# Kernel optimization log

Measured on AMD Instinct MI355X. Metric: run time of the kernel, lower is better.

## Reference

```python
import jax, jax.numpy as jnp
import numpy as np

LN_EPS = 1e-5


def setup_inputs() -> dict:
    key = jax.random.key(0)
    ks = jax.random.split(key, 6)
    B, S, Dv, Dk, A = 32, 2048, 1024, 1024, 1024
    meta_state = jax.random.normal(ks[0], (B, S, Dv), dtype=jnp.float32)
    hidden_previous = jax.random.normal(ks[1], (B, Dk), dtype=jnp.float32)
    # torch nn.Linear weights are [out_features, in_features]
    WK = jax.random.normal(ks[2], (A, Dv), dtype=jnp.float32) * (1.0 / np.sqrt(Dv))
    WQ = jax.random.normal(ks[3], (A, Dk), dtype=jnp.float32) * (1.0 / np.sqrt(Dk))
    WV = jax.random.normal(ks[4], (Dv, Dv), dtype=jnp.float32) * (1.0 / np.sqrt(Dv))
    WO = jax.random.normal(ks[5], (Dv, Dv), dtype=jnp.float32) * (1.0 / np.sqrt(Dv))
    ln_w = jnp.ones((Dv,), dtype=jnp.float32)
    ln_b = jnp.zeros((Dv,), dtype=jnp.float32)
    return {"meta_state": meta_state, "hidden_previous": hidden_previous,
            "WK": WK, "WQ": WQ, "WV": WV, "WO": WO, "ln_w": ln_w, "ln_b": ln_b}


def reference(meta_state, hidden_previous, WK, WQ, WV, WO, ln_w, ln_b):
    A = WK.shape[0]
    scale = 1.0 / jnp.sqrt(jnp.asarray(A, dtype=meta_state.dtype))
    # projections
    K = jnp.einsum('bsd,ad->bsa', meta_state, WK)          # [B,S,A]
    q = jnp.einsum('bd,ad->ba', hidden_previous, WQ)       # [B,A]
    V = jnp.einsum('bsd,ed->bse', meta_state, WV)          # [B,S,Dv]
    # single-query attention over sequence dim
    logits = jnp.einsum('bsa,ba->bs', K, q) * scale        # [B,S]
    weight = jax.nn.softmax(logits, axis=1)                # softmax over S (dim=1)
    attention = jnp.einsum('bse,bs->be', V, weight)        # [B,Dv]
    # output layer: Linear(no bias) -> Tanh -> LayerNorm (dropout = identity in eval)
    h = jnp.tanh(attention @ WO.T)
    mu = jnp.mean(h, axis=-1, keepdims=True)
    var = jnp.mean(jnp.square(h - mu), axis=-1, keepdims=True)
    out = (h - mu) / jnp.sqrt(var + LN_EPS) * ln_w + ln_b  # [B,Dv]
    return out, weight[..., None]                          # weight shape [B,S,1] as in torch
```

## Files before the change

### kernel.cpp

```cpp
#include <hip/hip_runtime.h>
#include <math.h>

#define B 32
#define S 2048
#define D 1024
#define CPB 64
#define CHROWS (S / CPB)
#define WROWS (CHROWS / 4)
#define ACH 16
#define SCALE (1.0f / 32.0f)
#define LN_EPS 1e-5f

__device__ __forceinline__ float wave_sum(float v) {
#pragma unroll
  for (int off = 32; off > 0; off >>= 1) v += __shfl_xor(v, off, 64);
  return v;
}

__global__ __launch_bounds__(256) void gemm_xw(const float* __restrict__ X,
                                               const float* __restrict__ W,
                                               float* __restrict__ Y,
                                               const int do_tanh) {
  const int t = threadIdx.x;
  const int b = t & 31;
  const int rr = (t >> 5) & 3;
  const int kh = t >> 7;
  const int r = blockIdx.x * 4 + rr;
  const float4* x4 = (const float4*)(X + (size_t)b * D + kh * (D / 2));
  const float4* w4 = (const float4*)(W + (size_t)r * D + kh * (D / 2));
  float acc = 0.f;
#pragma unroll 8
  for (int k = 0; k < D / 8; ++k) {
    float4 a = x4[k];
    float4 w = w4[k];
    acc += a.x * w.x + a.y * w.y + a.z * w.z + a.w * w.w;
  }
  __shared__ float part[256];
  part[t] = acc;
  __syncthreads();
  if (kh == 0) {
    float v = part[t] + part[t + 128];
    if (do_tanh) v = tanhf(v);
    Y[(size_t)b * D + r] = v;
  }
}

__global__ __launch_bounds__(256) void kq_partial(const float* __restrict__ q,
                                                  const float* __restrict__ WK,
                                                  float* __restrict__ kqp) {
  const int t = threadIdx.x, ac = blockIdx.x, bg = blockIdx.y;
  const int d0 = t * 4;
  float accx[8] = {}, accy[8] = {}, accz[8] = {}, accw[8] = {};
  const int a0 = ac * (1024 / ACH);
  for (int a = a0; a < a0 + (1024 / ACH); ++a) {
    float4 wk = *(const float4*)(WK + (size_t)a * D + d0);
#pragma unroll
    for (int j = 0; j < 8; ++j) {
      float qv = q[(size_t)(bg * 8 + j) * D + a];
      accx[j] += qv * wk.x;
      accy[j] += qv * wk.y;
      accz[j] += qv * wk.z;
      accw[j] += qv * wk.w;
    }
  }
#pragma unroll
  for (int j = 0; j < 8; ++j) {
    float4 o;
    o.x = accx[j]; o.y = accy[j]; o.z = accz[j]; o.w = accw[j];
    *(float4*)(kqp + ((size_t)ac * B + bg * 8 + j) * D + d0) = o;
  }
}

__global__ __launch_bounds__(64) void kq_reduce(const float* __restrict__ kqp,
                                                float* __restrict__ kq) {
  const int i4 = (blockIdx.x * 64 + threadIdx.x) * 4;
  float sx = 0.f, sy = 0.f, sz = 0.f, sw = 0.f;
  for (int c = 0; c < ACH; ++c) {
    float4 v = *(const float4*)(kqp + (size_t)c * (B * D) + i4);
    sx += v.x; sy += v.y; sz += v.z; sw += v.w;
  }
  float4 o;
  o.x = sx; o.y = sy; o.z = sz; o.w = sw;
  *(float4*)(kq + i4) = o;
}

__global__ __launch_bounds__(256) void attn_main(
    const float* __restrict__ meta, const float* __restrict__ kq,
    float* __restrict__ logits_out, float* __restrict__ cm,
    float* __restrict__ cl, float* __restrict__ cacc) {
  const int c = blockIdx.x, b = blockIdx.y;
  const int t = threadIdx.x, w = t >> 6, lane = t & 63;
  const int row0 = c * CHROWS + w * WROWS;
  const float* base = meta + ((size_t)b * S + row0) * D + lane * 4;

  float4 kqf[4];
#pragma unroll
  for (int j = 0; j < 4; ++j)
    kqf[j] = *(const float4*)(kq + (size_t)b * D + j * 256 + lane * 4);

  float4 acc[4] = {};
  float m = -INFINITY, l = 0.f;

  float4 v[4], vn[4];
#pragma unroll
  for (int j = 0; j < 4; ++j) v[j] = *(const float4*)(base + j * 256);

  for (int s = 0; s < WROWS; ++s) {
    const float* nb = base + (size_t)(s + 1 < WROWS ? s + 1 : s) * D;
#pragma unroll
    for (int j = 0; j < 4; ++j) vn[j] = *(const float4*)(nb + j * 256);

    float p = 0.f;
#pragma unroll
    for (int j = 0; j < 4; ++j)
      p += v[j].x * kqf[j].x + v[j].y * kqf[j].y + v[j].z * kqf[j].z +
           v[j].w * kqf[j].w;
    p = wave_sum(p);
    const float logit = p * SCALE;
    if (lane == 0) logits_out[(size_t)b * S + row0 + s] = logit;

    if (logit > m) {
      const float f = expf(m - logit);
#pragma unroll
      for (int j = 0; j < 4; ++j) {
        acc[j].x *= f; acc[j].y *= f; acc[j].z *= f; acc[j].w *= f;
      }
      l *= f;
      m = logit;
    }
    const float p2 = expf(logit - m);
#pragma unroll
    for (int j = 0; j < 4; ++j) {
      acc[j].x += p2 * v[j].x; acc[j].y += p2 * v[j].y;
      acc[j].z += p2 * v[j].z; acc[j].w += p2 * v[j].w;
    }
    l += p2;
#pragma unroll
    for (int j = 0; j < 4; ++j) v[j] = vn[j];
  }

  __shared__ float lds_acc[4][D];
  __shared__ float lds_m[4], lds_l[4];
  if (lane == 0) { lds_m[w] = m; lds_l[w] = l; }
#pragma unroll
  for (int j = 0; j < 4; ++j)
    *(float4*)(&lds_acc[w][j * 256 + lane * 4]) = acc[j];
  __syncthreads();

  const float M = fmaxf(fmaxf(lds_m[0], lds_m[1]), fmaxf(lds_m[2], lds_m[3]));
  float fac[4], L = 0.f;
#pragma unroll
  for (int w2 = 0; w2 < 4; ++w2) {
    fac[w2] = expf(lds_m[w2] - M);
    L += lds_l[w2] * fac[w2];
  }
  float4 sv = {};
#pragma unroll
  for (int w2 = 0; w2 < 4; ++w2) {
    float4 a = *(const float4*)(&lds_acc[w2][t * 4]);
    sv.x += fac[w2] * a.x; sv.y += fac[w2] * a.y;
    sv.z += fac[w2] * a.z; sv.w += fac[w2] * a.w;
  }
  const int pc = b * CPB + c;
  *(float4*)(cacc + (size_t)pc * D + t * 4) = sv;
  if (t == 0) { cm[pc] = M; cl[pc] = L; }
}

__global__ __launch_bounds__(128) void combine(const float* __restrict__ cm,
                                               const float* __restrict__ cl,
                                               const float* __restrict__ cacc,
                                               float* __restrict__ wio,
                                               float* __restrict__ wm) {
  const int b = blockIdx.x, dt = blockIdx.y, t = threadIdx.x;
  float M = -INFINITY;
  for (int c2 = 0; c2 < CPB; ++c2) M = fmaxf(M, cm[b * CPB + c2]);
  __shared__ float fac[CPB];
  if (t < CPB) fac[t] = expf(cm[b * CPB + t] - M);
  __syncthreads();
  float L = 0.f;
  for (int c2 = 0; c2 < CPB; ++c2) L += cl[b * CPB + c2] * fac[c2];
  const float invL = 1.0f / L;

  const int d = dt * 128 + t;
  float sv = 0.f;
  for (int c2 = 0; c2 < CPB; ++c2)
    sv += fac[c2] * cacc[((size_t)b * CPB + c2) * D + d];
  wm[(size_t)b * D + d] = sv * invL;

  for (int s = dt * 256 + t; s < dt * 256 + 256; s += 128) {
    const float lg = wio[(size_t)b * S + s];
    wio[(size_t)b * S + s] = expf(lg - M) * invL;
  }
}

__global__ __launch_bounds__(256) void ln_kernel(const float* __restrict__ h,
                                                 const float* __restrict__ lnw,
                                                 const float* __restrict__ lnb,
                                                 float* __restrict__ out) {
  const int b = blockIdx.x, t = threadIdx.x, wid = t >> 6, lane = t & 63;
  __shared__ float r1[4], r2[4];
  float4 v = *(const float4*)(h + (size_t)b * D + 4 * t);
  float s1 = v.x + v.y + v.z + v.w;
  float s2 = v.x * v.x + v.y * v.y + v.z * v.z + v.w * v.w;
  s1 = wave_sum(s1);
  s2 = wave_sum(s2);
  if (lane == 0) { r1[wid] = s1; r2[wid] = s2; }
  __syncthreads();
  const float mean = (r1[0] + r1[1] + r1[2] + r1[3]) * (1.0f / D);
  const float ms = (r2[0] + r2[1] + r2[2] + r2[3]) * (1.0f / D);
  const float var = ms - mean * mean;
  const float rstd = rsqrtf(var + LN_EPS);
  float4 w = *(const float4*)(lnw + 4 * t);
  float4 bb = *(const float4*)(lnb + 4 * t);
  float4 o;
  o.x = (v.x - mean) * rstd * w.x + bb.x;
  o.y = (v.y - mean) * rstd * w.y + bb.y;
  o.z = (v.z - mean) * rstd * w.z + bb.z;
  o.w = (v.w - mean) * rstd * w.w + bb.w;
  *(float4*)(out + (size_t)b * D + 4 * t) = o;
}

extern "C" void kernel_launch(void* const* d_in, const int* in_sizes, int n_in,
                              void* d_out, int out_size, void* d_ws,
                              size_t ws_size, hipStream_t stream) {
  (void)in_sizes; (void)n_in; (void)out_size; (void)ws_size;
  const float* meta   = (const float*)d_in[0];
  const float* hidden = (const float*)d_in[1];
  const float* WK = (const float*)d_in[2];
  const float* WQ = (const float*)d_in[3];
  const float* WV = (const float*)d_in[4];
  const float* WO = (const float*)d_in[5];
  const float* lnw = (const float*)d_in[6];
  const float* lnb = (const float*)d_in[7];

  float* out  = (float*)d_out;
  float* wout = out + B * D;

  float* ws   = (float*)d_ws;
  float* q    = ws;
  float* kqp  = q + B * D;
  float* kq   = kqp + (size_t)ACH * B * D;
  float* cm   = kq + B * D;
  float* cl   = cm + B * CPB;
  float* cacc = cl + B * CPB;
  float* wm   = cacc + (size_t)B * CPB * D;
  float* att  = wm + B * D;
  float* h    = att + B * D;

  gemm_xw<<<dim3(D / 4), 256, 0, stream>>>(hidden, WQ, q, 0);
  kq_partial<<<dim3(ACH, 4), 256, 0, stream>>>(q, WK, kqp);
  kq_reduce<<<dim3((B * D) / 256), 64, 0, stream>>>(kqp, kq);
  attn_main<<<dim3(CPB, B), 256, 0, stream>>>(meta, kq, wout, cm, cl, cacc);
  combine<<<dim3(B, 8), 128, 0, stream>>>(cm, cl, cacc, wout, wm);
  gemm_xw<<<dim3(D / 4), 256, 0, stream>>>(wm, WV, att, 0);
  gemm_xw<<<dim3(D / 4), 256, 0, stream>>>(att, WO, h, 1);
  ln_kernel<<<dim3(B), 256, 0, stream>>>(h, lnw, lnb, out);
}
```

Before: 475.6 us.

## Fuse kq reduction into attention, unroll rows by two, restructure small GEMMs

Removes the separate kq_reduce kernel: each attention block now sums the 16 partial kq chunks itself and stages the result through shared memory. The attention loop handles two sequence rows per iteration, sharing one wave reduction and one max/rescale step, and fast __expf replaces expf. The small GEMM kernel is rewritten so each wave owns one batch row, keeps x in registers and streams 32 weight rows with prefetch. The trade-off is redundant kqp reads by every attention block (64 per batch), higher register use, and slightly less accurate exponentials.

```diff
diff --git a/kernel.cpp b/kernel.cpp
--- a/kernel.cpp
+++ b/kernel.cpp
@@ -17,31 +17,50 @@
   return v;
 }
 
+__device__ __forceinline__ void wave_sum2(float& a, float& b) {
+#pragma unroll
+  for (int off = 32; off > 0; off >>= 1) {
+    a += __shfl_xor(a, off, 64);
+    b += __shfl_xor(b, off, 64);
+  }
+}
+
 __global__ __launch_bounds__(256) void gemm_xw(const float* __restrict__ X,
                                                const float* __restrict__ W,
                                                float* __restrict__ Y,
                                                const int do_tanh) {
-  const int t = threadIdx.x;
-  const int b = t & 31;
-  const int rr = (t >> 5) & 3;
-  const int kh = t >> 7;
-  const int r = blockIdx.x * 4 + rr;
-  const float4* x4 = (const float4*)(X + (size_t)b * D + kh * (D / 2));
-  const float4* w4 = (const float4*)(W + (size_t)r * D + kh * (D / 2));
-  float acc = 0.f;
-#pragma unroll 8
-  for (int k = 0; k < D / 8; ++k) {
-    float4 a = x4[k];
-    float4 w = w4[k];
-    acc += a.x * w.x + a.y * w.y + a.z * w.z + a.w * w.w;
-  }
-  __shared__ float part[256];
-  part[t] = acc;
-  __syncthreads();
-  if (kh == 0) {
-    float v = part[t] + part[t + 128];
-    if (do_tanh) v = tanhf(v);
-    Y[(size_t)b * D + r] = v;
+  const int w = threadIdx.x >> 6, lane = threadIdx.x & 63;
+  const int b = blockIdx.x * 4 + w;
+  const int r0 = blockIdx.y * 32;
+
+  float4 x[4];
+  const float4* xrow = (const float4*)(X + (size_t)b * D) + lane;
+#pragma unroll
+  for (int j = 0; j < 4; ++j) x[j] = xrow[j * 64];
+
+  float4 wv[4], wn[4];
+  const float4* wrow = (const float4*)(W + (size_t)r0 * D) + lane;
+#pragma unroll
+  for (int j = 0; j < 4; ++j) wv[j] = wrow[j * 64];
+
+  for (int i = 0; i < 32; ++i) {
+    const float4* wnext =
+        (const float4*)(W + (size_t)(r0 + (i + 1 < 32 ? i + 1 : i)) * D) + lane;
+#pragma unroll
+    for (int j = 0; j < 4; ++j) wn[j] = wnext[j * 64];
+
+    float p = 0.f;
+#pragma unroll
+    for (int j = 0; j < 4; ++j)
+      p += x[j].x * wv[j].x + x[j].y * wv[j].y + x[j].z * wv[j].z +
+           x[j].w * wv[j].w;
+    p = wave_sum(p);
+    if (lane == 0) {
+      if (do_tanh) p = tanhf(p);
+      Y[(size_t)b * D + r0 + i] = p;
+    }
+#pragma unroll
+    for (int j = 0; j < 4; ++j) wv[j] = wn[j];
   }
 }
 
@@ -71,21 +90,8 @@
   }
 }
 
-__global__ __launch_bounds__(64) void kq_reduce(const float* __restrict__ kqp,
-                                                float* __restrict__ kq) {
-  const int i4 = (blockIdx.x * 64 + threadIdx.x) * 4;
-  float sx = 0.f, sy = 0.f, sz = 0.f, sw = 0.f;
-  for (int c = 0; c < ACH; ++c) {
-    float4 v = *(const float4*)(kqp + (size_t)c * (B * D) + i4);
-    sx += v.x; sy += v.y; sz += v.z; sw += v.w;
-  }
-  float4 o;
-  o.x = sx; o.y = sy; o.z = sz; o.w = sw;
-  *(float4*)(kq + i4) = o;
-}
-
 __global__ __launch_bounds__(256) void attn_main(
-    const float* __restrict__ meta, const float* __restrict__ kq,
+    const float* __restrict__ meta, const float* __restrict__ kqp,
     float* __restrict__ logits_out, float* __restrict__ cm,
     float* __restrict__ cl, float* __restrict__ cacc) {
   const int c = blockIdx.x, b = blockIdx.y;
@@ -93,54 +99,87 @@
   const int row0 = c * CHROWS + w * WROWS;
   const float* base = meta + ((size_t)b * S + row0) * D + lane * 4;
 
+  __shared__ float lds_acc[4][D];
+  __shared__ float lds_m[4], lds_l[4];
+  float* kq_lds = &lds_acc[0][0];
+
+  {
+    float sx = 0.f, sy = 0.f, sz = 0.f, sw = 0.f;
+#pragma unroll
+    for (int ch = 0; ch < ACH; ++ch) {
+      float4 kv = *(const float4*)(kqp + ((size_t)ch * B + b) * D + 4 * t);
+      sx += kv.x; sy += kv.y; sz += kv.z; sw += kv.w;
+    }
+    float4 o;
+    o.x = sx; o.y = sy; o.z = sz; o.w = sw;
+    *(float4*)(&kq_lds[4 * t]) = o;
+  }
+
+  float4 v0[4], v1[4];
+#pragma unroll
+  for (int j = 0; j < 4; ++j) {
+    v0[j] = *(const float4*)(base + j * 256);
+    v1[j] = *(const float4*)(base + D + j * 256);
+  }
+
+  __syncthreads();
   float4 kqf[4];
 #pragma unroll
   for (int j = 0; j < 4; ++j)
-    kqf[j] = *(const float4*)(kq + (size_t)b * D + j * 256 + lane * 4);
+    kqf[j] = *(const float4*)(&kq_lds[j * 256 + lane * 4]);
+  __syncthreads();
 
   float4 acc[4] = {};
   float m = -INFINITY, l = 0.f;
 
-  float4 v[4], vn[4];
-#pragma unroll
-  for (int j = 0; j < 4; ++j) v[j] = *(const float4*)(base + j * 256);
-
-  for (int s = 0; s < WROWS; ++s) {
-    const float* nb = base + (size_t)(s + 1 < WROWS ? s + 1 : s) * D;
-#pragma unroll
-    for (int j = 0; j < 4; ++j) vn[j] = *(const float4*)(nb + j * 256);
-
-    float p = 0.f;
-#pragma unroll
-    for (int j = 0; j < 4; ++j)
-      p += v[j].x * kqf[j].x + v[j].y * kqf[j].y + v[j].z * kqf[j].z +
-           v[j].w * kqf[j].w;
-    p = wave_sum(p);
-    const float logit = p * SCALE;
-    if (lane == 0) logits_out[(size_t)b * S + row0 + s] = logit;
-
-    if (logit > m) {
-      const float f = expf(m - logit);
+  for (int it = 0; it < WROWS / 2; ++it) {
+    const int nr = (it + 1 < WROWS / 2) ? 2 * it + 2 : 2 * it;
+    const float* nb = base + (size_t)nr * D;
+    float4 n0[4], n1[4];
+#pragma unroll
+    for (int j = 0; j < 4; ++j) {
+      n0[j] = *(const float4*)(nb + j * 256);
+      n1[j] = *(const float4*)(nb + D + j * 256);
+    }
+
+    float pa = 0.f, pb = 0.f;
+#pragma unroll
+    for (int j = 0; j < 4; ++j) {
+      pa += v0[j].x * kqf[j].x + v0[j].y * kqf[j].y + v0[j].z * kqf[j].z +
+            v0[j].w * kqf[j].w;
+      pb += v1[j].x * kqf[j].x + v1[j].y * kqf[j].y + v1[j].z * kqf[j].z +
+            v1[j].w * kqf[j].w;
+    }
+    wave_sum2(pa, pb);
+    const float la = pa * SCALE, lb = pb * SCALE;
+    if (lane == 0) {
+      logits_out[(size_t)b * S + row0 + 2 * it] = la;
+      logits_out[(size_t)b * S + row0 + 2 * it + 1] = lb;
+    }
+
+    const float mn = fmaxf(m, fmaxf(la, lb));
+    if (mn > m) {
+      const float f = __expf(m - mn);
 #pragma unroll
       for (int j = 0; j < 4; ++j) {
         acc[j].x *= f; acc[j].y *= f; acc[j].z *= f; acc[j].w *= f;
       }
       l *= f;
-      m = logit;
-    }
-    const float p2 = expf(logit - m);
+      m = mn;
+    }
+    const float ea = __expf(la - m), eb = __expf(lb - m);
 #pragma unroll
     for (int j = 0; j < 4; ++j) {
-      acc[j].x += p2 * v[j].x; acc[j].y += p2 * v[j].y;
-      acc[j].z += p2 * v[j].z; acc[j].w += p2 * v[j].w;
-    }
-    l += p2;
-#pragma unroll
-    for (int j = 0; j < 4; ++j) v[j] = vn[j];
-  }
-
-  __shared__ float lds_acc[4][D];
-  __shared__ float lds_m[4], lds_l[4];
+      acc[j].x += ea * v0[j].x + eb * v1[j].x;
+      acc[j].y += ea * v0[j].y + eb * v1[j].y;
+      acc[j].z += ea * v0[j].z + eb * v1[j].z;
+      acc[j].w += ea * v0[j].w + eb * v1[j].w;
+    }
+    l += ea + eb;
+#pragma unroll
+    for (int j = 0; j < 4; ++j) { v0[j] = n0[j]; v1[j] = n1[j]; }
+  }
+
   if (lane == 0) { lds_m[w] = m; lds_l[w] = l; }
 #pragma unroll
   for (int j = 0; j < 4; ++j)
@@ -151,7 +190,7 @@
   float fac[4], L = 0.f;
 #pragma unroll
   for (int w2 = 0; w2 < 4; ++w2) {
-    fac[w2] = expf(lds_m[w2] - M);
+    fac[w2] = __expf(lds_m[w2] - M);
     L += lds_l[w2] * fac[w2];
   }
   float4 sv = {};
@@ -175,7 +214,7 @@
   float M = -INFINITY;
   for (int c2 = 0; c2 < CPB; ++c2) M = fmaxf(M, cm[b * CPB + c2]);
   __shared__ float fac[CPB];
-  if (t < CPB) fac[t] = expf(cm[b * CPB + t] - M);
+  if (t < CPB) fac[t] = __expf(cm[b * CPB + t] - M);
   __syncthreads();
   float L = 0.f;
   for (int c2 = 0; c2 < CPB; ++c2) L += cl[b * CPB + c2] * fac[c2];
@@ -189,7 +228,7 @@
 
   for (int s = dt * 256 + t; s < dt * 256 + 256; s += 128) {
     const float lg = wio[(size_t)b * S + s];
-    wio[(size_t)b * S + s] = expf(lg - M) * invL;
+    wio[(size_t)b * S + s] = __expf(lg - M) * invL;
   }
 }
 
@@ -239,20 +278,18 @@
   float* ws   = (float*)d_ws;
   float* q    = ws;
   float* kqp  = q + B * D;
-  float* kq   = kqp + (size_t)ACH * B * D;
-  float* cm   = kq + B * D;
+  float* cm   = kqp + (size_t)ACH * B * D;
   float* cl   = cm + B * CPB;
   float* cacc = cl + B * CPB;
   float* wm   = cacc + (size_t)B * CPB * D;
   float* att  = wm + B * D;
   float* h    = att + B * D;
 
-  gemm_xw<<<dim3(D / 4), 256, 0, stream>>>(hidden, WQ, q, 0);
+  gemm_xw<<<dim3(8, 32), 256, 0, stream>>>(hidden, WQ, q, 0);
   kq_partial<<<dim3(ACH, 4), 256, 0, stream>>>(q, WK, kqp);
-  kq_reduce<<<dim3((B * D) / 256), 64, 0, stream>>>(kqp, kq);
-  attn_main<<<dim3(CPB, B), 256, 0, stream>>>(meta, kq, wout, cm, cl, cacc);
+  attn_main<<<dim3(CPB, B), 256, 0, stream>>>(meta, kqp, wout, cm, cl, cacc);
   combine<<<dim3(B, 8), 128, 0, stream>>>(cm, cl, cacc, wout, wm);
-  gemm_xw<<<dim3(D / 4), 256, 0, stream>>>(wm, WV, att, 0);
-  gemm_xw<<<dim3(D / 4), 256, 0, stream>>>(att, WO, h, 1);
+  gemm_xw<<<dim3(8, 32), 256, 0, stream>>>(wm, WV, att, 0);
+  gemm_xw<<<dim3(8, 32), 256, 0, stream>>>(att, WO, h, 1);
   ln_kernel<<<dim3(B), 256, 0, stream>>>(h, lnw, lnb, out);
 }
```

Result: faster. 462.6 us (-2.7%).
